# Kernel optimization log

Measured on AMD Instinct MI355X. Metric: run time of the kernel, lower is better.

The kernel has to match this reference:

```python
import jax, jax.numpy as jnp
import numpy as np

N = 100000
E = 3200000


def setup_inputs() -> dict:
    key = jax.random.key(0)
    k1, k2, k3 = jax.random.split(key, 3)
    x = jax.random.normal(k1, (N, 256), dtype=jnp.float32)
    edge_index = jax.random.randint(k2, (2, E), 0, N, dtype=jnp.int64)
    W = jax.random.normal(k3, (256, 64), dtype=jnp.float32) * (1.0 / np.sqrt(256.0))
    b = jnp.zeros((64,), dtype=jnp.float32)
    return {"x": x, "edge_index": edge_index, "W": W, "b": b}


def reference(x, edge_index, W, b):
    # GCNConv (PyG defaults): add self-loops, symmetric deg normalization,
    # linear transform, neighbor aggregation, bias.
    n = x.shape[0]
    loops = jnp.arange(n, dtype=edge_index.dtype)
    row = jnp.concatenate([edge_index[0], loops])  # src
    col = jnp.concatenate([edge_index[1], loops])  # dst

    # degree over destination nodes (incl. self-loops)
    deg = jax.ops.segment_sum(jnp.ones_like(col, dtype=x.dtype), col, num_segments=n)
    deg_inv_sqrt = jnp.where(deg > 0, jax.lax.rsqrt(deg), 0.0)
    norm = deg_inv_sqrt[row] * deg_inv_sqrt[col]  # [E+N]

    h = x @ W  # [N, C]
    msgs = h[row] * norm[:, None]  # gather + scale
    out = jax.ops.segment_sum(msgs, col, num_segments=n)  # scatter-add
    return out + b
```

## Files before the change

### kernel.cpp

```cpp
#include <hip/hip_runtime.h>

#define C_IN 256
#define C_OUT 64
#define BSH 7
#define NPB 128
#define NB 1024
#define CHUNK 4096
#define ROWS 4

typedef short bf16x8 __attribute__((ext_vector_type(8)));
typedef float f32x4 __attribute__((ext_vector_type(4)));

__device__ __forceinline__ unsigned short f2bf(float f) {
    unsigned u = __builtin_bit_cast(unsigned, f);
    u = (u + 0x7FFFu + ((u >> 16) & 1u)) >> 16;
    return (unsigned short)u;
}
__device__ __forceinline__ float bflo(unsigned u) {
    return __builtin_bit_cast(float, u << 16);
}
__device__ __forceinline__ float bfhi(unsigned u) {
    return __builtin_bit_cast(float, u & 0xffff0000u);
}

__global__ __launch_bounds__(256) void k_wt(const float* __restrict__ W,
                                            unsigned short* __restrict__ WT) {
#pragma unroll
    for (int i = 0; i < 16; ++i) {
        int f = i * 256 + threadIdx.x;
        int k = f >> 4;
        int n4 = (f & 15) * 4;
        float4 v = ((const float4*)W)[f];
        WT[(n4 + 0) * 256 + k] = f2bf(v.x);
        WT[(n4 + 1) * 256 + k] = f2bf(v.y);
        WT[(n4 + 2) * 256 + k] = f2bf(v.z);
        WT[(n4 + 3) * 256 + k] = f2bf(v.w);
    }
}

__global__ __launch_bounds__(1024) void k_hist2(const int* __restrict__ dst,
                                                int* __restrict__ table, int e) {
    __shared__ int cnt[NB];
    if (threadIdx.x < NB) cnt[threadIdx.x] = 0;
    __syncthreads();
    int b0 = blockIdx.x * CHUNK;
#pragma unroll
    for (int k = 0; k < CHUNK / 1024; ++k) {
        int i = b0 + k * 1024 + threadIdx.x;
        if (i < e) atomicAdd(&cnt[dst[i] >> BSH], 1);
    }
    __syncthreads();
    if (threadIdx.x < NB) table[(size_t)blockIdx.x * NB + threadIdx.x] = cnt[threadIdx.x];
}

__global__ __launch_bounds__(256) void kA2(int* __restrict__ table,
                                           int* __restrict__ tot, int nbin) {
    __shared__ int part[256];
    int bucket = blockIdx.x;
    int t = threadIdx.x;
    int v[ROWS];
    int s = 0;
#pragma unroll
    for (int i = 0; i < ROWS; ++i) {
        int r = t * ROWS + i;
        int x = (r < nbin) ? table[(size_t)r * NB + bucket] : 0;
        v[i] = s;
        s += x;
    }
    part[t] = s;
    __syncthreads();
    for (int off = 1; off < 256; off <<= 1) {
        int u = (t >= off) ? part[t - off] : 0;
        __syncthreads();
        part[t] += u;
        __syncthreads();
    }
    int base = part[t] - s;
#pragma unroll
    for (int i = 0; i < ROWS; ++i) {
        int r = t * ROWS + i;
        if (r < nbin) table[(size_t)r * NB + bucket] = v[i] + base;
    }
    if (t == 255) tot[bucket] = part[255];
}

__global__ __launch_bounds__(1024) void kB(const int* __restrict__ tot,
                                           int* __restrict__ gbase, int e) {
    __shared__ int l[NB];
    int t = threadIdx.x;
    int v = tot[t];
    l[t] = v;
    __syncthreads();
    for (int off = 1; off < NB; off <<= 1) {
        int u = (t >= off) ? l[t - off] : 0;
        __syncthreads();
        l[t] += u;
        __syncthreads();
    }
    gbase[t] = l[t] - v;
    if (t == NB - 1) gbase[NB] = e;
}

__global__ __launch_bounds__(1024) void k_bin2(const int* __restrict__ src,
                                               const int* __restrict__ dst,
                                               const int* __restrict__ table,
                                               const int* __restrict__ gbase,
                                               int* __restrict__ sorted, int e) {
    __shared__ int cur[NB];
    if (threadIdx.x < NB)
        cur[threadIdx.x] = table[(size_t)blockIdx.x * NB + threadIdx.x] + gbase[threadIdx.x];
    __syncthreads();
    int b0 = blockIdx.x * CHUNK;
#pragma unroll
    for (int k = 0; k < CHUNK / 1024; ++k) {
        int i = b0 + k * 1024 + threadIdx.x;
        if (i < e) {
            int d = dst[i];
            int bb = d >> BSH;
            int off = atomicAdd(&cur[bb], 1);
            sorted[off] = (src[i] << BSH) | (d & (NPB - 1));
        }
    }
}

__global__ __launch_bounds__(512) void k_sort2(const int* __restrict__ sorted,
                                               const int* __restrict__ gbase,
                                               int* __restrict__ eidx,
                                               int* __restrict__ rowptr,
                                               float* __restrict__ dinv, int n, int e) {
    __shared__ int cnt[NPB];
    __shared__ int sc[NPB];
    __shared__ int cur[NPB];
    int b = blockIdx.x;
    int node0 = b * NPB;
    int range = min(NPB, n - node0);
    int inbase = gbase[b];
    int m_b = gbase[b + 1] - inbase;
    if (threadIdx.x < NPB) cnt[threadIdx.x] = 0;
    __syncthreads();
    for (int j = threadIdx.x; j < m_b; j += 512)
        atomicAdd(&cnt[sorted[inbase + j] & (NPB - 1)], 1);
    __syncthreads();
    if (threadIdx.x < NPB) sc[threadIdx.x] = cnt[threadIdx.x];
    __syncthreads();
    for (int off = 1; off < NPB; off <<= 1) {
        int t = (threadIdx.x < NPB && threadIdx.x >= off) ? sc[threadIdx.x - off] : 0;
        __syncthreads();
        if (threadIdx.x < NPB) sc[threadIdx.x] += t;
        __syncthreads();
    }
    if (threadIdx.x < NPB) {
        int excl = inbase + sc[threadIdx.x] - cnt[threadIdx.x];
        cur[threadIdx.x] = excl;
        if (threadIdx.x < range) {
            rowptr[node0 + threadIdx.x] = excl;
            dinv[node0 + threadIdx.x] = rsqrtf((float)(cnt[threadIdx.x] + 1));
        }
    }
    __syncthreads();
    for (int j = threadIdx.x; j < m_b; j += 512) {
        int v = sorted[inbase + j];
        int pos = atomicAdd(&cur[v & (NPB - 1)], 1);
        eidx[pos] = v >> BSH;
    }
    if (b == 0 && threadIdx.x == 0) rowptr[n] = e;
}

__global__ __launch_bounds__(256, 4) void k_gemm(const float* __restrict__ x,
                                                 const unsigned short* __restrict__ WT,
                                                 const float* __restrict__ dinv,
                                                 unsigned short* __restrict__ h, int n) {
    const int t = threadIdx.x;
    const int lane = t & 63;
    const int w = t >> 6;
    const int m = lane & 15;
    const int q = lane >> 4;

    int arow = blockIdx.x * 64 + 16 * w + m;
    const float* xr = x + (size_t)(arow < n ? arow : 0) * C_IN + q * 8;

    float4 raw[16];
#pragma unroll
    for (int ks = 0; ks < 8; ++ks) {
        raw[2 * ks]     = *(const float4*)&xr[ks * 32];
        raw[2 * ks + 1] = *(const float4*)&xr[ks * 32 + 4];
    }

    float di[4];
#pragma unroll
    for (int r = 0; r < 4; ++r) {
        int gr = blockIdx.x * 64 + 16 * w + q * 4 + r;
        di[r] = dinv[gr < n ? gr : 0];
    }

    bf16x8 A[8];
#pragma unroll
    for (int ks = 0; ks < 8; ++ks) {
        float4 v0 = raw[2 * ks];
        float4 v1 = raw[2 * ks + 1];
        bf16x8 a;
        a[0] = (short)f2bf(v0.x); a[1] = (short)f2bf(v0.y);
        a[2] = (short)f2bf(v0.z); a[3] = (short)f2bf(v0.w);
        a[4] = (short)f2bf(v1.x); a[5] = (short)f2bf(v1.y);
        a[6] = (short)f2bf(v1.z); a[7] = (short)f2bf(v1.w);
        A[ks] = a;
    }

    f32x4 acc[4];
#pragma unroll
    for (int nt = 0; nt < 4; ++nt) acc[nt] = (f32x4){0.f, 0.f, 0.f, 0.f};

    const unsigned short* wb = WT + (size_t)m * 256 + q * 8;
#pragma unroll
    for (int ks = 0; ks < 8; ++ks) {
#pragma unroll
        for (int nt = 0; nt < 4; ++nt) {
            bf16x8 B = *(const bf16x8*)&wb[nt * 16 * 256 + ks * 32];
            acc[nt] = __builtin_amdgcn_mfma_f32_16x16x32_bf16(A[ks], B, acc[nt], 0, 0, 0);
        }
    }

#pragma unroll
    for (int r = 0; r < 4; ++r) {
        int gr = blockIdx.x * 64 + 16 * w + q * 4 + r;
        if (gr < n) {
#pragma unroll
            for (int nt = 0; nt < 4; ++nt)
                h[(size_t)gr * C_OUT + nt * 16 + m] = f2bf(acc[nt][r] * di[r]);
        }
    }
}

__global__ __launch_bounds__(256) void k_gather(const int* __restrict__ rowptr,
                                                const int* __restrict__ eidx,
                                                const unsigned short* __restrict__ h,
                                                const float* __restrict__ dinv,
                                                const float* __restrict__ bias,
                                                float* __restrict__ out, int n) {
    int node = blockIdx.x * 4 + (threadIdx.x >> 6);
    if (node >= n) return;
    int lane = threadIdx.x & 63;
    int g = lane >> 3;
    int c8 = (lane & 7) * 8;

    int beg = rowptr[node];
    int end = rowptr[node + 1];
    float a0 = 0.f, a1 = 0.f, a2 = 0.f, a3 = 0.f;
    float a4 = 0.f, a5 = 0.f, a6 = 0.f, a7 = 0.f;

    int j = beg;
    for (; j + 15 < end; j += 16) {
        int sa = eidx[j + g];
        int sb = eidx[j + 8 + g];
        uint4 ha = *(const uint4*)&h[(size_t)sa * C_OUT + c8];
        uint4 hb = *(const uint4*)&h[(size_t)sb * C_OUT + c8];
        a0 += bflo(ha.x); a1 += bfhi(ha.x); a2 += bflo(ha.y); a3 += bfhi(ha.y);
        a4 += bflo(ha.z); a5 += bfhi(ha.z); a6 += bflo(ha.w); a7 += bfhi(ha.w);
        a0 += bflo(hb.x); a1 += bfhi(hb.x); a2 += bflo(hb.y); a3 += bfhi(hb.y);
        a4 += bflo(hb.z); a5 += bfhi(hb.z); a6 += bflo(hb.w); a7 += bfhi(hb.w);
    }
    for (; j < end; j += 8) {
        int rem = end - j;
        int idx = j + ((g < rem) ? g : 0);
        int s = eidx[idx];
        float mq = (g < rem) ? 1.f : 0.f;
        uint4 hv = *(const uint4*)&h[(size_t)s * C_OUT + c8];
        a0 += bflo(hv.x) * mq; a1 += bfhi(hv.x) * mq;
        a2 += bflo(hv.y) * mq; a3 += bfhi(hv.y) * mq;
        a4 += bflo(hv.z) * mq; a5 += bfhi(hv.z) * mq;
        a6 += bflo(hv.w) * mq; a7 += bfhi(hv.w) * mq;
    }
#pragma unroll
    for (int off = 8; off < 64; off <<= 1) {
        a0 += __shfl_xor(a0, off, 64); a1 += __shfl_xor(a1, off, 64);
        a2 += __shfl_xor(a2, off, 64); a3 += __shfl_xor(a3, off, 64);
        a4 += __shfl_xor(a4, off, 64); a5 += __shfl_xor(a5, off, 64);
        a6 += __shfl_xor(a6, off, 64); a7 += __shfl_xor(a7, off, 64);
    }
    if (g == 0) {
        float di = dinv[node];
        uint4 sv = *(const uint4*)&h[(size_t)node * C_OUT + c8];
        float4 b0 = *(const float4*)&bias[c8];
        float4 b1 = *(const float4*)&bias[c8 + 4];
        float4 o0, o1;
        o0.x = (a0 + bflo(sv.x)) * di + b0.x;
        o0.y = (a1 + bfhi(sv.x)) * di + b0.y;
        o0.z = (a2 + bflo(sv.y)) * di + b0.z;
        o0.w = (a3 + bfhi(sv.y)) * di + b0.w;
        o1.x = (a4 + bflo(sv.z)) * di + b1.x;
        o1.y = (a5 + bfhi(sv.z)) * di + b1.y;
        o1.z = (a6 + bflo(sv.w)) * di + b1.z;
        o1.w = (a7 + bfhi(sv.w)) * di + b1.w;
        *(float4*)&out[(size_t)node * C_OUT + c8] = o0;
        *(float4*)&out[(size_t)node * C_OUT + c8 + 4] = o1;
    }
}

extern "C" void kernel_launch(void* const* d_in, const int* in_sizes, int n_in,
                              void* d_out, int out_size, void* d_ws, size_t ws_size,
                              hipStream_t stream) {
    const float* x = (const float*)d_in[0];
    const int* ei = (const int*)d_in[1];
    const float* W = (const float*)d_in[2];
    const float* bias = (const float*)d_in[3];
    float* out = (float*)d_out;

    const int n = in_sizes[0] / C_IN;
    const int e = in_sizes[1] / 2;
    const int* src = ei;
    const int* dst = ei + e;

    const int nbin = (e + CHUNK - 1) / CHUNK;
    const int nbuck = (n + NPB - 1) / NPB;

    char* w = (char*)d_ws;
    unsigned short* h = (unsigned short*)w;  w += (size_t)n * C_OUT * 2;
    int* sorted = (int*)w;                   w += (size_t)e * 4;
    int* eidx = (int*)w;                     w += (size_t)e * 4;
    float* dinv = (float*)w;                 w += (size_t)n * 4;
    int* rowptr = (int*)w;                   w += (size_t)(n + 1) * 4;
    int* table = (int*)w;                    w += (size_t)nbin * NB * 4;
    int* tot = (int*)w;                      w += NB * 4;
    int* gbase = (int*)w;                    w += (NB + 1) * 4;
    unsigned short* WT = (unsigned short*)w; w += (size_t)C_OUT * C_IN * 2;

    k_wt<<<1, 256, 0, stream>>>(W, WT);
    k_hist2<<<nbin, 1024, 0, stream>>>(dst, table, e);
    kA2<<<NB, 256, 0, stream>>>(table, tot, nbin);
    kB<<<1, 1024, 0, stream>>>(tot, gbase, e);
    k_bin2<<<nbin, 1024, 0, stream>>>(src, dst, table, gbase, sorted, e);
    k_sort2<<<nbuck, 512, 0, stream>>>(sorted, gbase, eidx, rowptr, dinv, n, e);
    k_gemm<<<(n + 63) / 64, 256, 0, stream>>>(x, WT, dinv, h, n);
    k_gather<<<(n + 3) / 4, 256, 0, stream>>>(rowptr, eidx, h, dinv, bias, out, n);
}
```

Before: 353.7 us.

## Stage swizzled bf16 weights in LDS via direct global-to-LDS loads in GEMM

The weight transpose kernel now writes W^T in an XOR-swizzled layout. Each GEMM block copies the full 32KB weight tile into shared memory using global_load_lds, then reads the B fragments from LDS, where the swizzle avoids bank conflicts. This replaces repeated per-wave global/L2 reads of W. The x loads are issued as inline asm with an explicit waitcnt. In exchange it adds 32KB of LDS per block, lowers the occupancy hint from 4 to 3, and puts a block-wide barrier before compute.

Measured after the change: 337.5 us. 1.05x faster.

```diff
diff --git a/kernel.cpp b/kernel.cpp
--- a/kernel.cpp
+++ b/kernel.cpp
@@ -24,17 +24,20 @@
 }
 
 __global__ __launch_bounds__(256) void k_wt(const float* __restrict__ W,
-                                            unsigned short* __restrict__ WT) {
+                                            unsigned short* __restrict__ WTs) {
 #pragma unroll
     for (int i = 0; i < 16; ++i) {
         int f = i * 256 + threadIdx.x;
         int k = f >> 4;
         int n4 = (f & 15) * 4;
         float4 v = ((const float4*)W)[f];
-        WT[(n4 + 0) * 256 + k] = f2bf(v.x);
-        WT[(n4 + 1) * 256 + k] = f2bf(v.y);
-        WT[(n4 + 2) * 256 + k] = f2bf(v.z);
-        WT[(n4 + 3) * 256 + k] = f2bf(v.w);
+        int c = k >> 3, ci = k & 7;
+        float vv[4] = {v.x, v.y, v.z, v.w};
+#pragma unroll
+        for (int r = 0; r < 4; ++r) {
+            int row = n4 + r;
+            WTs[row * 256 + ((c ^ (row & 7)) << 3) + ci] = f2bf(vv[r]);
+        }
     }
 }
 
@@ -166,30 +169,47 @@
     if (b == 0 && threadIdx.x == 0) rowptr[n] = e;
 }
 
-__global__ __launch_bounds__(256, 4) void k_gemm(const float* __restrict__ x,
-                                                 const unsigned short* __restrict__ WT,
+__global__ __launch_bounds__(256, 3) void k_gemm(const float* __restrict__ x,
+                                                 const unsigned short* __restrict__ WTs,
                                                  const float* __restrict__ dinv,
                                                  unsigned short* __restrict__ h, int n) {
+    __shared__ unsigned short Wl[64 * 256];
+
     const int t = threadIdx.x;
     const int lane = t & 63;
-    const int w = t >> 6;
+    const int wv = t >> 6;
     const int m = lane & 15;
     const int q = lane >> 4;
-
-    int arow = blockIdx.x * 64 + 16 * w + m;
-    const float* xr = x + (size_t)(arow < n ? arow : 0) * C_IN + q * 8;
-
+    const int mx = m & 7;
+
+#pragma unroll
+    for (int j = 0; j < 8; ++j) {
+        const unsigned short* gsrc = WTs + j * 2048 + wv * 512 + lane * 8;
+        unsigned short* ldst = Wl + j * 2048 + wv * 512;
+        __builtin_amdgcn_global_load_lds(
+            (const __attribute__((address_space(1))) unsigned int*)gsrc,
+            (__attribute__((address_space(3))) unsigned int*)ldst, 16, 0, 0);
+    }
+
+    int arow = blockIdx.x * 64 + 16 * wv + m;
+    const float* xp = x + (size_t)(arow < n ? arow : 0) * C_IN + q * 8;
     float4 raw[16];
 #pragma unroll
     for (int ks = 0; ks < 8; ++ks) {
-        raw[2 * ks]     = *(const float4*)&xr[ks * 32];
-        raw[2 * ks + 1] = *(const float4*)&xr[ks * 32 + 4];
-    }
+        const float* p0 = xp + ks * 32;
+        const float* p1 = xp + ks * 32 + 4;
+        asm volatile("global_load_dwordx4 %0, %1, off" : "=v"(raw[2 * ks]) : "v"(p0));
+        asm volatile("global_load_dwordx4 %0, %1, off" : "=v"(raw[2 * ks + 1]) : "v"(p1));
+    }
+
+    asm volatile("s_waitcnt vmcnt(0)" ::: "memory");
+    __builtin_amdgcn_sched_barrier(0);
+    __syncthreads();
 
     float di[4];
 #pragma unroll
     for (int r = 0; r < 4; ++r) {
-        int gr = blockIdx.x * 64 + 16 * w + q * 4 + r;
+        int gr = blockIdx.x * 64 + 16 * wv + q * 4 + r;
         di[r] = dinv[gr < n ? gr : 0];
     }
 
@@ -210,19 +230,20 @@
 #pragma unroll
     for (int nt = 0; nt < 4; ++nt) acc[nt] = (f32x4){0.f, 0.f, 0.f, 0.f};
 
-    const unsigned short* wb = WT + (size_t)m * 256 + q * 8;
 #pragma unroll
     for (int ks = 0; ks < 8; ++ks) {
+        int c = ks * 4 + q;
+        int cs = (c ^ mx) << 3;
 #pragma unroll
         for (int nt = 0; nt < 4; ++nt) {
-            bf16x8 B = *(const bf16x8*)&wb[nt * 16 * 256 + ks * 32];
+            bf16x8 B = *(const bf16x8*)&Wl[(nt * 16 + m) * 256 + cs];
             acc[nt] = __builtin_amdgcn_mfma_f32_16x16x32_bf16(A[ks], B, acc[nt], 0, 0, 0);
         }
     }
 
 #pragma unroll
     for (int r = 0; r < 4; ++r) {
-        int gr = blockIdx.x * 64 + 16 * w + q * 4 + r;
+        int gr = blockIdx.x * 64 + 16 * wv + q * 4 + r;
         if (gr < n) {
 #pragma unroll
             for (int nt = 0; nt < 4; ++nt)
@@ -322,14 +343,14 @@
     int* table = (int*)w;                    w += (size_t)nbin * NB * 4;
     int* tot = (int*)w;                      w += NB * 4;
     int* gbase = (int*)w;                    w += (NB + 1) * 4;
-    unsigned short* WT = (unsigned short*)w; w += (size_t)C_OUT * C_IN * 2;
-
-    k_wt<<<1, 256, 0, stream>>>(W, WT);
+    unsigned short* WTs = (unsigned short*)w; w += (size_t)C_OUT * C_IN * 2;
+
+    k_wt<<<1, 256, 0, stream>>>(W, WTs);
     k_hist2<<<nbin, 1024, 0, stream>>>(dst, table, e);
     kA2<<<NB, 256, 0, stream>>>(table, tot, nbin);
     kB<<<1, 1024, 0, stream>>>(tot, gbase, e);
     k_bin2<<<nbin, 1024, 0, stream>>>(src, dst, table, gbase, sorted, e);
     k_sort2<<<nbuck, 512, 0, stream>>>(sorted, gbase, eidx, rowptr, dinv, n, e);
-    k_gemm<<<(n + 63) / 64, 256, 0, stream>>>(x, WT, dinv, h, n);
+    k_gemm<<<(n + 63) / 64, 256, 0, stream>>>(x, WTs, dinv, h, n);
     k_gather<<<(n + 3) / 4, 256, 0, stream>>>(rowptr, eidx, h, dinv, bias, out, n);
 }
```
